# Optimization experiments

Measured on AMD Instinct MI355X. Metric: run time of the kernel, lower is better.

## Reference

```python
import jax, jax.numpy as jnp
import numpy as np

L, B, S, D, H = 4, 4, 2048, 512, 8
DH = D // H
FF = 4 * D
BN_EPS = 1e-3  # keras BatchNormalization default epsilon


def setup_inputs() -> dict:
    key = jax.random.key(0)
    ks = jax.random.split(key, 8)
    g = lambda k, shape: jax.random.normal(k, shape, dtype=jnp.float32) * 0.02
    return {
        "sequence": jax.random.normal(ks[0], (B, S, D), dtype=jnp.float32),
        "wq": g(ks[1], (L, D, D)), "bq": jnp.zeros((L, D), jnp.float32),
        "wk": g(ks[2], (L, D, D)), "bk": jnp.zeros((L, D), jnp.float32),
        "wv": g(ks[3], (L, D, D)), "bv": jnp.zeros((L, D), jnp.float32),
        "wo": g(ks[4], (L, D, D)), "bo": jnp.zeros((L, D), jnp.float32),
        "w1": g(ks[5], (L, D, FF)), "b1": jnp.zeros((L, FF), jnp.float32),
        "w2": g(ks[6], (L, FF, D)), "b2": jnp.zeros((L, D), jnp.float32),
        "g1": jnp.ones((L, D), jnp.float32), "be1": jnp.zeros((L, D), jnp.float32),
        "g2": jnp.ones((L, D), jnp.float32), "be2": jnp.zeros((L, D), jnp.float32),
    }


def reference(sequence, wq, bq, wk, bk, wv, bv, wo, bo, w1, b1, w2, b2, g1, be1, g2, be2):
    # Inference-mode BatchNorm with moving_mean=0, moving_var=1:
    # bn(x) = x / sqrt(1 + eps) * gamma + beta
    bn_inv = 1.0 / jnp.sqrt(jnp.float32(1.0 + BN_EPS))
    scale = 1.0 / jnp.sqrt(jnp.float32(DH))
    x = sequence  # [B, S, D]
    for i in range(L):
        # Batched multi-head self-attention (== the per-position loop concat)
        q = (x @ wq[i] + bq[i]).reshape(B, S, H, DH)
        k = (x @ wk[i] + bk[i]).reshape(B, S, H, DH)
        v = (x @ wv[i] + bv[i]).reshape(B, S, H, DH)
        att = jax.nn.softmax(jnp.einsum('bqhd,bkhd->bhqk', q, k) * scale, axis=-1)
        o = jnp.einsum('bhqk,bkhd->bqhd', att, v).reshape(B, S, D)
        o = o @ wo[i] + bo[i]
        x = (x + o) * bn_inv * g1[i] + be1[i]          # residual + BN
        f = jax.nn.relu(x @ w1[i] + b1[i]) @ w2[i] + b2[i]  # FFN
        x = (x + f) * bn_inv * g2[i] + be2[i]          # residual + BN
    return x
```

## Files before the change

### kernel.cpp

```cpp
#include <hip/hip_runtime.h>
#include <hip/hip_bf16.h>

#define BB   4
#define SS   2048
#define DDIM 512
#define HH   8
#define DHD  64
#define FFD  2048
#define LLN  4
#define NQKV 1536
#define BN_INV 0.9995003747f
#define QSCALE 0.18033688011112042f

typedef __bf16 bf16x8 __attribute__((ext_vector_type(8)));
typedef __bf16 bf16x4 __attribute__((ext_vector_type(4)));
typedef float  f32x4  __attribute__((ext_vector_type(4)));
typedef float  f32x16 __attribute__((ext_vector_type(16)));

__device__ __forceinline__ void gl2lds16(const void* g, void* l) {
  __builtin_amdgcn_global_load_lds((const __attribute__((address_space(1))) void*)g,
                                   (__attribute__((address_space(3))) void*)l, 16, 0, 0);
}

__device__ __forceinline__ unsigned pkbf16(float a, float b) {
  union { __bf16 h[2]; unsigned u; } x;
  x.h[0] = (__bf16)a; x.h[1] = (__bf16)b;
  return x.u;
}

#define SBAR() do { __builtin_amdgcn_s_barrier(); asm volatile("" ::: "memory"); } while (0)

__global__ __launch_bounds__(256) void k_transpose_w(const float* __restrict__ in,
                                                     __bf16* __restrict__ out,
                                                     int R, int C,
                                                     size_t in_zs, size_t out_zs) {
  __shared__ float tile[32][33];
  in += (size_t)blockIdx.z * in_zs;
  out += (size_t)blockIdx.z * out_zs;
  const int c0 = blockIdx.x * 32, r0 = blockIdx.y * 32;
  const int tx = threadIdx.x & 31, ty = threadIdx.x >> 5;
#pragma unroll
  for (int k = 0; k < 4; ++k) {
    int r = ty + k * 8;
    tile[r][tx] = in[(size_t)(r0 + r) * C + (c0 + tx)];
  }
  __syncthreads();
#pragma unroll
  for (int k = 0; k < 4; ++k) {
    int c = ty + k * 8;
    out[(size_t)(c0 + c) * R + (r0 + tx)] = (__bf16)tile[tx][c];
  }
}

__global__ __launch_bounds__(256) void k_bias_fuse(const float* __restrict__ bq,
                                                   const float* __restrict__ bk,
                                                   const float* __restrict__ bv,
                                                   float* __restrict__ out) {
  const int i = blockIdx.x * 256 + threadIdx.x;
  const int l = i / NQKV, j = i - l * NQKV;
  float v = (j < 512) ? bq[l * 512 + j]
          : (j < 1024) ? bk[l * 512 + j - 512]
                       : bv[l * 512 + j - 1024];
  out[i] = v;
}

__global__ __launch_bounds__(256) void k_transpose_v(const __bf16* __restrict__ qkv,
                                                     __bf16* __restrict__ vt) {
  __shared__ __bf16 tile[32][33];
  const int s0 = blockIdx.x * 32;
  const int d0 = blockIdx.y * 32;
  const int bh = blockIdx.z, b = bh >> 3, h = bh & 7;
  const int tx = threadIdx.x & 31, ty = threadIdx.x >> 5;
#pragma unroll
  for (int k = 0; k < 4; ++k) {
    int s = ty + k * 8;
    tile[s][tx] = qkv[(size_t)(b * SS + s0 + s) * NQKV + 2 * DDIM + h * DHD + d0 + tx];
  }
  __syncthreads();
#pragma unroll
  for (int k = 0; k < 4; ++k) {
    int d = ty + k * 8;
    vt[(size_t)(bh * DHD + d0 + d) * SS + (s0 + tx)] = tile[tx][d];
  }
}

__global__ __launch_bounds__(256) void k_cast(const float* __restrict__ in,
                                              float* __restrict__ xf,
                                              __bf16* __restrict__ xb) {
  const int i = (blockIdx.x * 256 + threadIdx.x) * 4;
  const float4 v = *(const float4*)(in + i);
  *(float4*)(xf + i) = v;
  bf16x4 o;
  o[0] = (__bf16)v.x; o[1] = (__bf16)v.y; o[2] = (__bf16)v.z; o[3] = (__bf16)v.w;
  *(bf16x4*)(xb + i) = o;
}

template <int EPI>
__global__ __launch_bounds__(256) void k_gemm_bt(const __bf16* __restrict__ A,
                                                 const __bf16* __restrict__ Bt,
                                                 const float* __restrict__ bias,
                                                 __bf16* __restrict__ Cb,
                                                 int M, int N, int K,
                                                 const float* __restrict__ xres,
                                                 float* __restrict__ xout,
                                                 const float* __restrict__ gvec,
                                                 const float* __restrict__ bvec) {
  __shared__ __align__(16) char As[2][16384];
  __shared__ __align__(16) char Bs[2][16384];
  const int tid = threadIdx.x;
  const int l = tid & 63, w = tid >> 6;
  const int wm = w >> 1, wn = w & 1;
  const int m0 = blockIdx.y * 128, n0 = blockIdx.x * 128;
  const int lr = l & 15, lg = l >> 4;
  f32x4 acc[4][4] = {};
  const int nk = K >> 6;
  const size_t ldab = (size_t)K * 2;

  auto stage = [&](int buf, int kt) {
    const int k0b = kt * 128;
#pragma unroll
    for (int i = 0; i < 4; ++i) {
      const int chunk = i * 256 + tid;
      const int row = chunk >> 3;
      const int scb = ((chunk & 7) * 16) ^ ((row & 7) << 4);
      gl2lds16((const char*)A + (size_t)(m0 + row) * ldab + k0b + scb,
               As[buf] + (i * 256 + w * 64) * 16);
      gl2lds16((const char*)Bt + (size_t)(n0 + row) * ldab + k0b + scb,
               Bs[buf] + (i * 256 + w * 64) * 16);
    }
  };

  stage(0, 0);
  __syncthreads();
  int cur = 0;
  for (int kt = 0; kt < nk; ++kt) {
    if (kt + 1 < nk) stage(cur ^ 1, kt + 1);
#pragma unroll
    for (int kk = 0; kk < 2; ++kk) {
      bf16x8 a[4], b[4];
#pragma unroll
      for (int m = 0; m < 4; ++m) {
        const int row = wm * 64 + m * 16 + lr;
        const int cb = kk * 64 + lg * 16;
        a[m] = *(const bf16x8*)(As[cur] + row * 128 + (cb ^ ((row & 7) << 4)));
      }
#pragma unroll
      for (int n = 0; n < 4; ++n) {
        const int row = wn * 64 + n * 16 + lr;
        const int cb = kk * 64 + lg * 16;
        b[n] = *(const bf16x8*)(Bs[cur] + row * 128 + (cb ^ ((row & 7) << 4)));
      }
#pragma unroll
      for (int m = 0; m < 4; ++m)
#pragma unroll
        for (int n = 0; n < 4; ++n)
          acc[m][n] = __builtin_amdgcn_mfma_f32_16x16x32_bf16(a[m], b[n], acc[m][n], 0, 0, 0);
    }
    asm volatile("s_waitcnt vmcnt(0)" ::: "memory");
    __syncthreads();
    cur ^= 1;
  }
#pragma unroll
  for (int m = 0; m < 4; ++m) {
    const int gm = m0 + wm * 64 + m * 16 + lg * 4;
#pragma unroll
    for (int n = 0; n < 4; ++n) {
      const int gn = n0 + wn * 64 + n * 16 + lr;
      const float bv_ = bias[gn];
#pragma unroll
      for (int j = 0; j < 4; ++j) {
        const size_t idx = (size_t)(gm + j) * N + gn;
        float v = acc[m][n][j] + bv_;
        if constexpr (EPI == 1) {
          Cb[idx] = (__bf16)fmaxf(v, 0.0f);
        } else if constexpr (EPI == 2) {
          float t = (xres[idx] + v) * BN_INV * gvec[gn] + bvec[gn];
          xout[idx] = t;
          Cb[idx] = (__bf16)t;
        } else {
          if (gn < DDIM) v *= QSCALE;
          Cb[idx] = (__bf16)v;
        }
      }
    }
  }
}

template <int EPI>
__global__ __launch_bounds__(512, 1) void k_gemm256(const __bf16* __restrict__ A,
                                                    const __bf16* __restrict__ Bt,
                                                    const float* __restrict__ bias,
                                                    __bf16* __restrict__ Cb,
                                                    int M, int N, int K) {
  __shared__ __align__(16) char As[2][32768];
  __shared__ __align__(16) char Bs[2][32768];
  const int tid = threadIdx.x;
  const int l = tid & 63, w = tid >> 6;
  const int wm = w >> 2, wn = w & 3;
  const int m0 = blockIdx.y * 256, n0 = blockIdx.x * 256;
  const int lr = l & 15, lg = l >> 4;
  f32x4 acc[8][4] = {};
  const int nk = K >> 6;
  const size_t ldab = (size_t)K * 2;

  auto stA = [&](int buf, int kt, int h) {
    const int k0b = kt * 128;
#pragma unroll
    for (int i = 0; i < 2; ++i) {
      const int chunk = h * 1024 + i * 512 + tid;
      const int row = chunk >> 3;
      const int scb = ((chunk & 7) * 16) ^ ((row & 7) << 4);
      gl2lds16((const char*)A + (size_t)(m0 + row) * ldab + k0b + scb,
               As[buf] + (h * 1024 + i * 512 + w * 64) * 16);
    }
  };
  auto stB = [&](int buf, int kt, int h) {
    const int k0b = kt * 128;
#pragma unroll
    for (int i = 0; i < 2; ++i) {
      const int chunk = h * 1024 + i * 512 + tid;
      const int row = chunk >> 3;
      const int scb = ((chunk & 7) * 16) ^ ((row & 7) << 4);
      gl2lds16((const char*)Bt + (size_t)(n0 + row) * ldab + k0b + scb,
               Bs[buf] + (h * 1024 + i * 512 + w * 64) * 16);
    }
  };

  stA(0, 0, 0); stA(0, 0, 1); stB(0, 0, 0); stB(0, 0, 1);
  asm volatile("s_waitcnt vmcnt(0)" ::: "memory");
  SBAR();

  int cur = 0;
  for (int kt = 0; kt < nk; ++kt) {
    const char* Ac = As[cur];
    const char* Bc = Bs[cur];
    const int oth = cur ^ 1;
    const bool pf = (kt + 1 < nk);
    bf16x8 af[4][2], bfr[4][2];
#pragma unroll
    for (int mi = 0; mi < 4; ++mi) {
      const int row = wm * 128 + mi * 16 + lr;
      const int swz = (row & 7) << 4;
#pragma unroll
      for (int kk = 0; kk < 2; ++kk)
        af[mi][kk] = *(const bf16x8*)(Ac + row * 128 + ((kk * 64 + lg * 16) ^ swz));
    }
#pragma unroll
    for (int ni = 0; ni < 2; ++ni) {
      const int row = wn * 64 + ni * 16 + lr;
      const int swz = (row & 7) << 4;
#pragma unroll
      for (int kk = 0; kk < 2; ++kk)
        bfr[ni][kk] = *(const bf16x8*)(Bc + row * 128 + ((kk * 64 + lg * 16) ^ swz));
    }
    if (pf) { stA(oth, kt + 1, 0); stA(oth, kt + 1, 1); }
    SBAR();
    __builtin_amdgcn_s_setprio(1);
#pragma unroll
    for (int mi = 0; mi < 4; ++mi)
#pragma unroll
      for (int ni = 0; ni < 2; ++ni)
#pragma unroll
        for (int kk = 0; kk < 2; ++kk)
          acc[mi][ni] = __builtin_amdgcn_mfma_f32_16x16x32_bf16(af[mi][kk], bfr[ni][kk], acc[mi][ni], 0, 0, 0);
    __builtin_amdgcn_s_setprio(0);
    SBAR();
#pragma unroll
    for (int ni = 2; ni < 4; ++ni) {
      const int row = wn * 64 + ni * 16 + lr;
      const int swz = (row & 7) << 4;
#pragma unroll
      for (int kk = 0; kk < 2; ++kk)
        bfr[ni][kk] = *(const bf16x8*)(Bc + row * 128 + ((kk * 64 + lg * 16) ^ swz));
    }
    if (pf) { stB(oth, kt + 1, 0); stB(oth, kt + 1, 1); }
    SBAR();
    __builtin_amdgcn_s_setprio(1);
#pragma unroll
    for (int mi = 0; mi < 4; ++mi)
#pragma unroll
      for (int ni = 2; ni < 4; ++ni)
#pragma unroll
        for (int kk = 0; kk < 2; ++kk)
          acc[mi][ni] = __builtin_amdgcn_mfma_f32_16x16x32_bf16(af[mi][kk], bfr[ni][kk], acc[mi][ni], 0, 0, 0);
    __builtin_amdgcn_s_setprio(0);
    SBAR();
#pragma unroll
    for (int mi = 0; mi < 4; ++mi) {
      const int row = wm * 128 + (mi + 4) * 16 + lr;
      const int swz = (row & 7) << 4;
#pragma unroll
      for (int kk = 0; kk < 2; ++kk)
        af[mi][kk] = *(const bf16x8*)(Ac + row * 128 + ((kk * 64 + lg * 16) ^ swz));
    }
    SBAR();
    __builtin_amdgcn_s_setprio(1);
#pragma unroll
    for (int mi = 0; mi < 4; ++mi)
#pragma unroll
      for (int ni = 0; ni < 2; ++ni)
#pragma unroll
        for (int kk = 0; kk < 2; ++kk)
          acc[mi + 4][ni] = __builtin_amdgcn_mfma_f32_16x16x32_bf16(af[mi][kk], bfr[ni][kk], acc[mi + 4][ni], 0, 0, 0);
    __builtin_amdgcn_s_setprio(0);
    SBAR();
    __builtin_amdgcn_s_setprio(1);
#pragma unroll
    for (int mi = 0; mi < 4; ++mi)
#pragma unroll
      for (int ni = 2; ni < 4; ++ni)
#pragma unroll
        for (int kk = 0; kk < 2; ++kk)
          acc[mi + 4][ni] = __builtin_amdgcn_mfma_f32_16x16x32_bf16(af[mi][kk], bfr[ni][kk], acc[mi + 4][ni], 0, 0, 0);
    __builtin_amdgcn_s_setprio(0);
    asm volatile("s_waitcnt vmcnt(0)" ::: "memory");
    SBAR();
    cur ^= 1;
  }
#pragma unroll
  for (int mi = 0; mi < 8; ++mi) {
    const int gm = m0 + wm * 128 + mi * 16 + lg * 4;
#pragma unroll
    for (int ni = 0; ni < 4; ++ni) {
      const int gn = n0 + wn * 64 + ni * 16 + lr;
      const float bv_ = bias[gn];
#pragma unroll
      for (int j = 0; j < 4; ++j) {
        const size_t idx = (size_t)(gm + j) * N + gn;
        float v = acc[mi][ni][j] + bv_;
        if constexpr (EPI == 1) {
          Cb[idx] = (__bf16)fmaxf(v, 0.0f);
        } else {
          if (gn < DDIM) v *= QSCALE;
          Cb[idx] = (__bf16)v;
        }
      }
    }
  }
}

__global__ __launch_bounds__(256, 2) void k_attn(const __bf16* __restrict__ QKV,
                                                 const __bf16* __restrict__ Vt,
                                                 __bf16* __restrict__ O) {
  __shared__ char smem[65536];
  const int tid = threadIdx.x, l = tid & 63, w = tid >> 6;
  const int lq = l & 31, hi = l >> 5;
  const int f = blockIdx.y * 16 + blockIdx.x;
  const int L = (f & 7) * 64 + (f >> 3);
  const int qt = L & 15, bh = L >> 4;
  const int b = bh >> 3, h = bh & 7;
  const int myq = qt * 128 + w * 32 + lq;
  bf16x8 qf[4];
  {
    const __bf16* qp = QKV + (size_t)(b * SS + myq) * NQKV + h * DHD + hi * 8;
#pragma unroll
    for (int kc = 0; kc < 4; ++kc)
      qf[kc] = *(const bf16x8*)(qp + kc * 16);
  }
  f32x16 oaccT[2] = {};
  float rsum = 0.f;

  auto stage = [&](int buf, int t) {
    const int kv0 = t * 128;
    char* Kd = smem + buf * 16384;
    char* Vd = smem + 32768 + buf * 16384;
#pragma unroll
    for (int i = 0; i < 4; ++i) {
      const int chunk = i * 256 + tid;
      const int row = chunk >> 3;
      const int rs = row ^ ((((row >> 2) + 1) & 2) * 6);
      const int scb = ((chunk & 7) * 16) ^ ((row & 7) << 4);
      gl2lds16((const char*)QKV + ((size_t)(b * SS + kv0 + rs) * NQKV + DDIM + h * DHD) * 2 + scb,
               Kd + (i * 256 + w * 64) * 16);
    }
#pragma unroll
    for (int i = 0; i < 4; ++i) {
      const int chunk = i * 256 + tid;
      const int row = chunk >> 4;
      const int scb = ((chunk & 15) * 16) ^ ((row & 15) << 4);
      gl2lds16((const char*)Vt + ((size_t)(bh * DHD + row) * SS + kv0) * 2 + scb,
               Vd + (i * 256 + w * 64) * 16);
    }
  };

  stage(0, 0);
  __syncthreads();
  int cur = 0;
  for (int t = 0; t < SS / 128; ++t) {
    if (t < SS / 128 - 1) stage(cur ^ 1, t + 1);
    const char* Ks = smem + cur * 16384;
    const char* Vs = smem + 32768 + cur * 16384;
#pragma unroll
    for (int kt2 = 0; kt2 < 4; ++kt2) {
      const int krow = kt2 * 32 + lq;
      const int kswz = (krow & 7) << 4;
      f32x16 st = {};
      __builtin_amdgcn_s_setprio(1);
#pragma unroll
      for (int kc = 0; kc < 4; ++kc) {
        bf16x8 kf = *(const bf16x8*)(Ks + krow * 128 + ((kc * 32 + hi * 16) ^ kswz));
        st = __builtin_amdgcn_mfma_f32_32x32x16_bf16(kf, qf[kc], st, 0, 0, 0);
      }
      __builtin_amdgcn_s_setprio(0);
      unsigned pk8[8];
#pragma unroll
      for (int i = 0; i < 8; ++i) {
        const float e0 = __builtin_amdgcn_exp2f(st[2 * i]);
        const float e1 = __builtin_amdgcn_exp2f(st[2 * i + 1]);
        rsum += e0 + e1;
        pk8[i] = pkbf16(e0, e1);
      }
      union { unsigned u[4]; bf16x8 v; } pf0, pf1;
#pragma unroll
      for (int i = 0; i < 4; ++i) { pf0.u[i] = pk8[i]; pf1.u[i] = pk8[4 + i]; }
      __builtin_amdgcn_s_setprio(1);
#pragma unroll
      for (int dt = 0; dt < 2; ++dt) {
        const int vrow = dt * 32 + lq;
        const int vswz = (vrow & 15) << 4;
        bf16x8 vf0 = *(const bf16x8*)(Vs + vrow * 256 + ((kt2 * 64 + hi * 16) ^ vswz));
        bf16x8 vf1 = *(const bf16x8*)(Vs + vrow * 256 + ((kt2 * 64 + 32 + hi * 16) ^ vswz));
        oaccT[dt] = __builtin_amdgcn_mfma_f32_32x32x16_bf16(vf0, pf0.v, oaccT[dt], 0, 0, 0);
        oaccT[dt] = __builtin_amdgcn_mfma_f32_32x32x16_bf16(vf1, pf1.v, oaccT[dt], 0, 0, 0);
      }
      __builtin_amdgcn_s_setprio(0);
    }
    asm volatile("s_waitcnt vmcnt(0)" ::: "memory");
    __syncthreads();
    cur ^= 1;
  }
  rsum += __shfl_xor(rsum, 32);
  const float inv = 1.0f / rsum;
  __bf16* op = O + (size_t)(b * SS + myq) * DDIM + h * DHD;
#pragma unroll
  for (int dt = 0; dt < 2; ++dt)
#pragma unroll
    for (int g = 0; g < 4; ++g) {
      const int d0 = dt * 32 + g * 8 + hi * 4;
      unsigned u0 = pkbf16(oaccT[dt][4 * g + 0] * inv, oaccT[dt][4 * g + 1] * inv);
      unsigned u1 = pkbf16(oaccT[dt][4 * g + 2] * inv, oaccT[dt][4 * g + 3] * inv);
      uint2 uu; uu.x = u0; uu.y = u1;
      *(uint2*)(op + d0) = uu;
    }
}

static constexpr size_t SZ_WQKVT = (size_t)LLN * NQKV * DDIM * 2;
static constexpr size_t SZ_WOT   = (size_t)LLN * DDIM * DDIM * 2;
static constexpr size_t SZ_WT_DF = (size_t)LLN * DDIM * FFD * 2;
static constexpr size_t SZ_BQKV  = (size_t)LLN * NQKV * 4;
static constexpr size_t SZ_X     = (size_t)BB * SS * DDIM * 4;
static constexpr size_t SZ_ABF   = (size_t)BB * SS * DDIM * 2;
static constexpr size_t SZ_QKV   = (size_t)BB * SS * NQKV * 2;
static constexpr size_t OFF_WQKVT = 0;
static constexpr size_t OFF_WOT  = OFF_WQKVT + SZ_WQKVT;
static constexpr size_t OFF_W1T  = OFF_WOT + SZ_WOT;
static constexpr size_t OFF_W2T  = OFF_W1T + SZ_WT_DF;
static constexpr size_t OFF_BQKV = OFF_W2T + SZ_WT_DF;
static constexpr size_t OFF_X    = OFF_BQKV + SZ_BQKV;
static constexpr size_t OFF_XB   = OFF_X + SZ_X;
static constexpr size_t OFF_QKV  = OFF_XB + SZ_ABF;
static constexpr size_t OFF_VT   = OFF_QKV + SZ_QKV;
static constexpr size_t OFF_OB   = OFF_VT + SZ_ABF;
static constexpr size_t OFF_H1   = OFF_QKV;

extern "C" void kernel_launch(void* const* d_in, const int* in_sizes, int n_in,
                              void* d_out, int out_size, void* d_ws, size_t ws_size,
                              hipStream_t stream) {
  const float* seq = (const float*)d_in[0];
  const float* wq = (const float*)d_in[1];  const float* bq = (const float*)d_in[2];
  const float* wk = (const float*)d_in[3];  const float* bk = (const float*)d_in[4];
  const float* wv = (const float*)d_in[5];  const float* bv = (const float*)d_in[6];
  const float* wo = (const float*)d_in[7];  const float* bo = (const float*)d_in[8];
  const float* w1 = (const float*)d_in[9];  const float* b1 = (const float*)d_in[10];
  const float* w2 = (const float*)d_in[11]; const float* b2 = (const float*)d_in[12];
  const float* g1 = (const float*)d_in[13]; const float* be1 = (const float*)d_in[14];
  const float* g2 = (const float*)d_in[15]; const float* be2 = (const float*)d_in[16];

  char* ws = (char*)d_ws;
  __bf16* wqkvt = (__bf16*)(ws + OFF_WQKVT);
  __bf16* wot = (__bf16*)(ws + OFF_WOT);
  __bf16* w1t = (__bf16*)(ws + OFF_W1T);
  __bf16* w2t = (__bf16*)(ws + OFF_W2T);
  float*  bqkv = (float*)(ws + OFF_BQKV);
  float*  xf  = (float*)(ws + OFF_X);
  __bf16* xb  = (__bf16*)(ws + OFF_XB);
  __bf16* qkvb = (__bf16*)(ws + OFF_QKV);
  __bf16* vtb = (__bf16*)(ws + OFF_VT);
  __bf16* ob  = (__bf16*)(ws + OFF_OB);
  __bf16* h1  = (__bf16*)(ws + OFF_H1);

  const size_t zDD = (size_t)DDIM * DDIM;
  const size_t zQKV = (size_t)NQKV * DDIM;
  const size_t zDF = (size_t)DDIM * FFD;
  k_transpose_w<<<dim3(16, 16, LLN), 256, 0, stream>>>(wq, wqkvt, DDIM, DDIM, zDD, zQKV);
  k_transpose_w<<<dim3(16, 16, LLN), 256, 0, stream>>>(wk, wqkvt + (size_t)DDIM * DDIM, DDIM, DDIM, zDD, zQKV);
  k_transpose_w<<<dim3(16, 16, LLN), 256, 0, stream>>>(wv, wqkvt + (size_t)2 * DDIM * DDIM, DDIM, DDIM, zDD, zQKV);
  k_transpose_w<<<dim3(16, 16, LLN), 256, 0, stream>>>(wo, wot, DDIM, DDIM, zDD, zDD);
  k_transpose_w<<<dim3(64, 16, LLN), 256, 0, stream>>>(w1, w1t, DDIM, FFD, zDF, zDF);
  k_transpose_w<<<dim3(16, 64, LLN), 256, 0, stream>>>(w2, w2t, FFD, DDIM, zDF, zDF);
  k_bias_fuse<<<LLN * NQKV / 256, 256, 0, stream>>>(bq, bk, bv, bqkv);
  k_cast<<<4096, 256, 0, stream>>>(seq, xf, xb);

  const int M = BB * SS;
  for (int i = 0; i < LLN; ++i) {
    k_gemm256<3><<<dim3(NQKV / 256, M / 256), 512, 0, stream>>>(
        xb, wqkvt + (size_t)i * NQKV * DDIM, bqkv + i * NQKV, qkvb, M, NQKV, DDIM);
    k_transpose_v<<<dim3(SS / 32, DHD / 32, BB * HH), 256, 0, stream>>>(qkvb, vtb);
    k_attn<<<dim3(SS / 128, BB * HH), 256, 0, stream>>>(qkvb, vtb, ob);
    k_gemm_bt<2><<<dim3(DDIM / 128, M / 128), 256, 0, stream>>>(
        ob, wot + (size_t)i * DDIM * DDIM, bo + i * DDIM, xb, M, DDIM, DDIM,
        xf, xf, g1 + i * DDIM, be1 + i * DDIM);
    k_gemm256<1><<<dim3(FFD / 256, M / 256), 512, 0, stream>>>(
        xb, w1t + (size_t)i * DDIM * FFD, b1 + i * FFD, h1, M, FFD, DDIM);
    k_gemm_bt<2><<<dim3(DDIM / 128, M / 128), 256, 0, stream>>>(
        h1, w2t + (size_t)i * DDIM * FFD, b2 + i * DDIM, xb, M, DDIM, FFD,
        xf, (i == LLN - 1) ? (float*)d_out : xf, g2 + i * DDIM, be2 + i * DDIM);
  }
  (void)in_sizes; (void)n_in; (void)out_size; (void)ws_size;
}
```

Baseline: 641.4 us.

## Process two query sub-tiles per wave in attention to reuse K/V fragments

```diff
diff --git a/kernel.cpp b/kernel.cpp
--- a/kernel.cpp
+++ b/kernel.cpp
@@ -339,9 +339,9 @@
   }
 }
 
-__global__ __launch_bounds__(256, 2) void k_attn(const __bf16* __restrict__ QKV,
-                                                 const __bf16* __restrict__ Vt,
-                                                 __bf16* __restrict__ O) {
+__global__ __launch_bounds__(128) void k_attn(const __bf16* __restrict__ QKV,
+                                              const __bf16* __restrict__ Vt,
+                                              __bf16* __restrict__ O) {
   __shared__ char smem[65536];
   const int tid = threadIdx.x, l = tid & 63, w = tid >> 6;
   const int lq = l & 31, hi = l >> 5;
@@ -349,37 +349,38 @@
   const int L = (f & 7) * 64 + (f >> 3);
   const int qt = L & 15, bh = L >> 4;
   const int b = bh >> 3, h = bh & 7;
-  const int myq = qt * 128 + w * 32 + lq;
-  bf16x8 qf[4];
-  {
-    const __bf16* qp = QKV + (size_t)(b * SS + myq) * NQKV + h * DHD + hi * 8;
+  const int q0 = qt * 128 + w * 64;
+  bf16x8 qf[2][4];
+#pragma unroll
+  for (int qh = 0; qh < 2; ++qh) {
+    const __bf16* qp = QKV + (size_t)(b * SS + q0 + qh * 32 + lq) * NQKV + h * DHD + hi * 8;
 #pragma unroll
     for (int kc = 0; kc < 4; ++kc)
-      qf[kc] = *(const bf16x8*)(qp + kc * 16);
-  }
-  f32x16 oaccT[2] = {};
-  float rsum = 0.f;
+      qf[qh][kc] = *(const bf16x8*)(qp + kc * 16);
+  }
+  f32x16 oaccT[2][2] = {};
+  float rsum[2] = {0.f, 0.f};
 
   auto stage = [&](int buf, int t) {
     const int kv0 = t * 128;
     char* Kd = smem + buf * 16384;
     char* Vd = smem + 32768 + buf * 16384;
 #pragma unroll
-    for (int i = 0; i < 4; ++i) {
-      const int chunk = i * 256 + tid;
+    for (int i = 0; i < 8; ++i) {
+      const int chunk = i * 128 + tid;
       const int row = chunk >> 3;
       const int rs = row ^ ((((row >> 2) + 1) & 2) * 6);
       const int scb = ((chunk & 7) * 16) ^ ((row & 7) << 4);
       gl2lds16((const char*)QKV + ((size_t)(b * SS + kv0 + rs) * NQKV + DDIM + h * DHD) * 2 + scb,
-               Kd + (i * 256 + w * 64) * 16);
-    }
-#pragma unroll
-    for (int i = 0; i < 4; ++i) {
-      const int chunk = i * 256 + tid;
+               Kd + (i * 128 + w * 64) * 16);
+    }
+#pragma unroll
+    for (int i = 0; i < 8; ++i) {
+      const int chunk = i * 128 + tid;
       const int row = chunk >> 4;
       const int scb = ((chunk & 15) * 16) ^ ((row & 15) << 4);
       gl2lds16((const char*)Vt + ((size_t)(bh * DHD + row) * SS + kv0) * 2 + scb,
-               Vd + (i * 256 + w * 64) * 16);
+               Vd + (i * 128 + w * 64) * 16);
     }
   };
 
@@ -394,25 +395,29 @@
     for (int kt2 = 0; kt2 < 4; ++kt2) {
       const int krow = kt2 * 32 + lq;
       const int kswz = (krow & 7) << 4;
-      f32x16 st = {};
+      f32x16 st0 = {}, st1 = {};
       __builtin_amdgcn_s_setprio(1);
 #pragma unroll
       for (int kc = 0; kc < 4; ++kc) {
         bf16x8 kf = *(const bf16x8*)(Ks + krow * 128 + ((kc * 32 + hi * 16) ^ kswz));
-        st = __builtin_amdgcn_mfma_f32_32x32x16_bf16(kf, qf[kc], st, 0, 0, 0);
+        st0 = __builtin_amdgcn_mfma_f32_32x32x16_bf16(kf, qf[0][kc], st0, 0, 0, 0);
+        st1 = __builtin_amdgcn_mfma_f32_32x32x16_bf16(kf, qf[1][kc], st1, 0, 0, 0);
       }
       __builtin_amdgcn_s_setprio(0);
-      unsigned pk8[8];
+      union { unsigned u[4]; bf16x8 v; } pf0[2], pf1[2];
 #pragma unroll
       for (int i = 0; i < 8; ++i) {
-        const float e0 = __builtin_amdgcn_exp2f(st[2 * i]);
-        const float e1 = __builtin_amdgcn_exp2f(st[2 * i + 1]);
-        rsum += e0 + e1;
-        pk8[i] = pkbf16(e0, e1);
-      }
-      union { unsigned u[4]; bf16x8 v; } pf0, pf1;
-#pragma unroll
-      for (int i = 0; i < 4; ++i) { pf0.u[i] = pk8[i]; pf1.u[i] = pk8[4 + i]; }
+        const float a0 = __builtin_amdgcn_exp2f(st0[2 * i]);
+        const float a1 = __builtin_amdgcn_exp2f(st0[2 * i + 1]);
+        rsum[0] += a0 + a1;
+        const unsigned ua = pkbf16(a0, a1);
+        if (i < 4) pf0[0].u[i] = ua; else pf1[0].u[i - 4] = ua;
+        const float c0 = __builtin_amdgcn_exp2f(st1[2 * i]);
+        const float c1 = __builtin_amdgcn_exp2f(st1[2 * i + 1]);
+        rsum[1] += c0 + c1;
+        const unsigned uc = pkbf16(c0, c1);
+        if (i < 4) pf0[1].u[i] = uc; else pf1[1].u[i - 4] = uc;
+      }
       __builtin_amdgcn_s_setprio(1);
 #pragma unroll
       for (int dt = 0; dt < 2; ++dt) {
@@ -420,8 +425,11 @@
         const int vswz = (vrow & 15) << 4;
         bf16x8 vf0 = *(const bf16x8*)(Vs + vrow * 256 + ((kt2 * 64 + hi * 16) ^ vswz));
         bf16x8 vf1 = *(const bf16x8*)(Vs + vrow * 256 + ((kt2 * 64 + 32 + hi * 16) ^ vswz));
-        oaccT[dt] = __builtin_amdgcn_mfma_f32_32x32x16_bf16(vf0, pf0.v, oaccT[dt], 0, 0, 0);
-        oaccT[dt] = __builtin_amdgcn_mfma_f32_32x32x16_bf16(vf1, pf1.v, oaccT[dt], 0, 0, 0);
+#pragma unroll
+        for (int qh = 0; qh < 2; ++qh) {
+          oaccT[dt][qh] = __builtin_amdgcn_mfma_f32_32x32x16_bf16(vf0, pf0[qh].v, oaccT[dt][qh], 0, 0, 0);
+          oaccT[dt][qh] = __builtin_amdgcn_mfma_f32_32x32x16_bf16(vf1, pf1[qh].v, oaccT[dt][qh], 0, 0, 0);
+        }
       }
       __builtin_amdgcn_s_setprio(0);
     }
@@ -429,19 +437,23 @@
     __syncthreads();
     cur ^= 1;
   }
-  rsum += __shfl_xor(rsum, 32);
-  const float inv = 1.0f / rsum;
-  __bf16* op = O + (size_t)(b * SS + myq) * DDIM + h * DHD;
-#pragma unroll
-  for (int dt = 0; dt < 2; ++dt)
-#pragma unroll
-    for (int g = 0; g < 4; ++g) {
-      const int d0 = dt * 32 + g * 8 + hi * 4;
-      unsigned u0 = pkbf16(oaccT[dt][4 * g + 0] * inv, oaccT[dt][4 * g + 1] * inv);
-      unsigned u1 = pkbf16(oaccT[dt][4 * g + 2] * inv, oaccT[dt][4 * g + 3] * inv);
-      uint2 uu; uu.x = u0; uu.y = u1;
-      *(uint2*)(op + d0) = uu;
-    }
+#pragma unroll
+  for (int qh = 0; qh < 2; ++qh) {
+    float v = rsum[qh];
+    v += __shfl_xor(v, 32);
+    const float inv = 1.0f / v;
+    __bf16* op = O + (size_t)(b * SS + q0 + qh * 32 + lq) * DDIM + h * DHD;
+#pragma unroll
+    for (int dt = 0; dt < 2; ++dt)
+#pragma unroll
+      for (int g = 0; g < 4; ++g) {
+        const int d0 = dt * 32 + g * 8 + hi * 4;
+        unsigned u0 = pkbf16(oaccT[dt][qh][4 * g + 0] * inv, oaccT[dt][qh][4 * g + 1] * inv);
+        unsigned u1 = pkbf16(oaccT[dt][qh][4 * g + 2] * inv, oaccT[dt][qh][4 * g + 3] * inv);
+        uint2 uu; uu.x = u0; uu.y = u1;
+        *(uint2*)(op + d0) = uu;
+      }
+  }
 }
 
 static constexpr size_t SZ_WQKVT = (size_t)LLN * NQKV * DDIM * 2;
@@ -506,7 +518,7 @@
     k_gemm256<3><<<dim3(NQKV / 256, M / 256), 512, 0, stream>>>(
         xb, wqkvt + (size_t)i * NQKV * DDIM, bqkv + i * NQKV, qkvb, M, NQKV, DDIM);
     k_transpose_v<<<dim3(SS / 32, DHD / 32, BB * HH), 256, 0, stream>>>(qkvb, vtb);
-    k_attn<<<dim3(SS / 128, BB * HH), 256, 0, stream>>>(qkvb, vtb, ob);
+    k_attn<<<dim3(SS / 128, BB * HH), 128, 0, stream>>>(qkvb, vtb, ob);
     k_gemm_bt<2><<<dim3(DDIM / 128, M / 128), 256, 0, stream>>>(
         ob, wot + (size_t)i * DDIM * DDIM, bo + i * DDIM, xb, M, DDIM, DDIM,
         xf, xf, g1 + i * DDIM, be1 + i * DDIM);
```

After: 684.2 us. 6.7% more time.

## Single-buffer K tile in attention to fit three blocks per CU

Applied to the files above, without the earlier changes.

```diff
diff --git a/kernel.cpp b/kernel.cpp
--- a/kernel.cpp
+++ b/kernel.cpp
@@ -339,10 +339,10 @@
   }
 }
 
-__global__ __launch_bounds__(256, 2) void k_attn(const __bf16* __restrict__ QKV,
+__global__ __launch_bounds__(256, 3) void k_attn(const __bf16* __restrict__ QKV,
                                                  const __bf16* __restrict__ Vt,
                                                  __bf16* __restrict__ O) {
-  __shared__ char smem[65536];
+  __shared__ char smem[49152];
   const int tid = threadIdx.x, l = tid & 63, w = tid >> 6;
   const int lq = l & 31, hi = l >> 5;
   const int f = blockIdx.y * 16 + blockIdx.x;
@@ -360,10 +360,8 @@
   f32x16 oaccT[2] = {};
   float rsum = 0.f;
 
-  auto stage = [&](int buf, int t) {
+  auto stageK = [&](int t) {
     const int kv0 = t * 128;
-    char* Kd = smem + buf * 16384;
-    char* Vd = smem + 32768 + buf * 16384;
 #pragma unroll
     for (int i = 0; i < 4; ++i) {
       const int chunk = i * 256 + tid;
@@ -371,8 +369,12 @@
       const int rs = row ^ ((((row >> 2) + 1) & 2) * 6);
       const int scb = ((chunk & 7) * 16) ^ ((row & 7) << 4);
       gl2lds16((const char*)QKV + ((size_t)(b * SS + kv0 + rs) * NQKV + DDIM + h * DHD) * 2 + scb,
-               Kd + (i * 256 + w * 64) * 16);
-    }
+               smem + (i * 256 + w * 64) * 16);
+    }
+  };
+  auto stageV = [&](int buf, int t) {
+    const int kv0 = t * 128;
+    char* Vd = smem + 16384 + buf * 16384;
 #pragma unroll
     for (int i = 0; i < 4; ++i) {
       const int chunk = i * 256 + tid;
@@ -383,36 +385,41 @@
     }
   };
 
-  stage(0, 0);
-  __syncthreads();
-  int cur = 0;
+  stageK(0); stageV(0, 0);
+  asm volatile("s_waitcnt vmcnt(0)" ::: "memory");
+  SBAR();
+  int vcur = 0;
   for (int t = 0; t < SS / 128; ++t) {
-    if (t < SS / 128 - 1) stage(cur ^ 1, t + 1);
-    const char* Ks = smem + cur * 16384;
-    const char* Vs = smem + 32768 + cur * 16384;
+    const char* Vs = smem + 16384 + vcur * 16384;
+    f32x16 st[4];
+    __builtin_amdgcn_s_setprio(1);
 #pragma unroll
     for (int kt2 = 0; kt2 < 4; ++kt2) {
       const int krow = kt2 * 32 + lq;
       const int kswz = (krow & 7) << 4;
-      f32x16 st = {};
-      __builtin_amdgcn_s_setprio(1);
+      f32x16 z = {};
 #pragma unroll
       for (int kc = 0; kc < 4; ++kc) {
-        bf16x8 kf = *(const bf16x8*)(Ks + krow * 128 + ((kc * 32 + hi * 16) ^ kswz));
-        st = __builtin_amdgcn_mfma_f32_32x32x16_bf16(kf, qf[kc], st, 0, 0, 0);
-      }
-      __builtin_amdgcn_s_setprio(0);
-      unsigned pk8[8];
+        bf16x8 kf = *(const bf16x8*)(smem + krow * 128 + ((kc * 32 + hi * 16) ^ kswz));
+        z = __builtin_amdgcn_mfma_f32_32x32x16_bf16(kf, qf[kc], z, 0, 0, 0);
+      }
+      st[kt2] = z;
+    }
+    __builtin_amdgcn_s_setprio(0);
+    asm volatile("s_waitcnt vmcnt(0)" ::: "memory");
+    SBAR();
+    if (t + 1 < SS / 128) { stageK(t + 1); stageV(vcur ^ 1, t + 1); }
+#pragma unroll
+    for (int kt2 = 0; kt2 < 4; ++kt2) {
+      union { unsigned u[4]; bf16x8 v; } pf0, pf1;
 #pragma unroll
       for (int i = 0; i < 8; ++i) {
-        const float e0 = __builtin_amdgcn_exp2f(st[2 * i]);
-        const float e1 = __builtin_amdgcn_exp2f(st[2 * i + 1]);
+        const float e0 = __builtin_amdgcn_exp2f(st[kt2][2 * i]);
+        const float e1 = __builtin_amdgcn_exp2f(st[kt2][2 * i + 1]);
         rsum += e0 + e1;
-        pk8[i] = pkbf16(e0, e1);
-      }
-      union { unsigned u[4]; bf16x8 v; } pf0, pf1;
-#pragma unroll
-      for (int i = 0; i < 4; ++i) { pf0.u[i] = pk8[i]; pf1.u[i] = pk8[4 + i]; }
+        const unsigned u = pkbf16(e0, e1);
+        if (i < 4) pf0.u[i] = u; else pf1.u[i - 4] = u;
+      }
       __builtin_amdgcn_s_setprio(1);
 #pragma unroll
       for (int dt = 0; dt < 2; ++dt) {
@@ -425,9 +432,11 @@
       }
       __builtin_amdgcn_s_setprio(0);
     }
-    asm volatile("s_waitcnt vmcnt(0)" ::: "memory");
-    __syncthreads();
-    cur ^= 1;
+    if (t + 1 < SS / 128) {
+      asm volatile("s_waitcnt vmcnt(4)" ::: "memory");
+    }
+    SBAR();
+    vcur ^= 1;
   }
   rsum += __shfl_xor(rsum, 32);
   const float inv = 1.0f / rsum;
```

New measurement: 651.3 us. About the same (+1.5%).

## Fuse V transpose into QKV GEMM epilogue and keep residual stream in bf16

Applied to the files above, without the earlier changes.

```diff
diff --git a/kernel.cpp b/kernel.cpp
--- a/kernel.cpp
+++ b/kernel.cpp
@@ -64,32 +64,10 @@
   out[i] = v;
 }
 
-__global__ __launch_bounds__(256) void k_transpose_v(const __bf16* __restrict__ qkv,
-                                                     __bf16* __restrict__ vt) {
-  __shared__ __bf16 tile[32][33];
-  const int s0 = blockIdx.x * 32;
-  const int d0 = blockIdx.y * 32;
-  const int bh = blockIdx.z, b = bh >> 3, h = bh & 7;
-  const int tx = threadIdx.x & 31, ty = threadIdx.x >> 5;
-#pragma unroll
-  for (int k = 0; k < 4; ++k) {
-    int s = ty + k * 8;
-    tile[s][tx] = qkv[(size_t)(b * SS + s0 + s) * NQKV + 2 * DDIM + h * DHD + d0 + tx];
-  }
-  __syncthreads();
-#pragma unroll
-  for (int k = 0; k < 4; ++k) {
-    int d = ty + k * 8;
-    vt[(size_t)(bh * DHD + d0 + d) * SS + (s0 + tx)] = tile[tx][d];
-  }
-}
-
 __global__ __launch_bounds__(256) void k_cast(const float* __restrict__ in,
-                                              float* __restrict__ xf,
                                               __bf16* __restrict__ xb) {
   const int i = (blockIdx.x * 256 + threadIdx.x) * 4;
   const float4 v = *(const float4*)(in + i);
-  *(float4*)(xf + i) = v;
   bf16x4 o;
   o[0] = (__bf16)v.x; o[1] = (__bf16)v.y; o[2] = (__bf16)v.z; o[3] = (__bf16)v.w;
   *(bf16x4*)(xb + i) = o;
@@ -99,9 +77,9 @@
 __global__ __launch_bounds__(256) void k_gemm_bt(const __bf16* __restrict__ A,
                                                  const __bf16* __restrict__ Bt,
                                                  const float* __restrict__ bias,
-                                                 __bf16* __restrict__ Cb,
+                                                 __bf16* Cb,
                                                  int M, int N, int K,
-                                                 const float* __restrict__ xres,
+                                                 const __bf16* xres,
                                                  float* __restrict__ xout,
                                                  const float* __restrict__ gvec,
                                                  const float* __restrict__ bvec) {
@@ -173,13 +151,10 @@
         float v = acc[m][n][j] + bv_;
         if constexpr (EPI == 1) {
           Cb[idx] = (__bf16)fmaxf(v, 0.0f);
-        } else if constexpr (EPI == 2) {
-          float t = (xres[idx] + v) * BN_INV * gvec[gn] + bvec[gn];
-          xout[idx] = t;
+        } else {
+          float t = ((float)xres[idx] + v) * BN_INV * gvec[gn] + bvec[gn];
+          if (xout) xout[idx] = t;
           Cb[idx] = (__bf16)t;
-        } else {
-          if (gn < DDIM) v *= QSCALE;
-          Cb[idx] = (__bf16)v;
         }
       }
     }
@@ -191,7 +166,8 @@
                                                     const __bf16* __restrict__ Bt,
                                                     const float* __restrict__ bias,
                                                     __bf16* __restrict__ Cb,
-                                                    int M, int N, int K) {
+                                                    int M, int N, int K,
+                                                    __bf16* __restrict__ vt) {
   __shared__ __align__(16) char As[2][32768];
   __shared__ __align__(16) char Bs[2][32768];
   const int tid = threadIdx.x;
@@ -317,23 +293,39 @@
     SBAR();
     cur ^= 1;
   }
+  const int bidx = m0 >> 11;
 #pragma unroll
   for (int mi = 0; mi < 8; ++mi) {
     const int gm = m0 + wm * 128 + mi * 16 + lg * 4;
 #pragma unroll
     for (int ni = 0; ni < 4; ++ni) {
-      const int gn = n0 + wn * 64 + ni * 16 + lr;
+      const int gnb = n0 + wn * 64 + ni * 16;
+      const int gn = gnb + lr;
       const float bv_ = bias[gn];
-#pragma unroll
-      for (int j = 0; j < 4; ++j) {
-        const size_t idx = (size_t)(gm + j) * N + gn;
-        float v = acc[mi][ni][j] + bv_;
-        if constexpr (EPI == 1) {
-          Cb[idx] = (__bf16)fmaxf(v, 0.0f);
-        } else {
-          if (gn < DDIM) v *= QSCALE;
-          Cb[idx] = (__bf16)v;
+      if (EPI == 1 || gnb < 2 * DDIM) {
+#pragma unroll
+        for (int j = 0; j < 4; ++j) {
+          const size_t idx = (size_t)(gm + j) * N + gn;
+          float v = acc[mi][ni][j] + bv_;
+          if constexpr (EPI == 1) {
+            Cb[idx] = (__bf16)fmaxf(v, 0.0f);
+          } else {
+            if (gn < DDIM) v *= QSCALE;
+            Cb[idx] = (__bf16)v;
+          }
         }
+      } else {
+        const int d = gn - 2 * DDIM;
+        const int h = d >> 6, dh = d & 63;
+        const int sbase = gm & 2047;
+        const float v0 = acc[mi][ni][0] + bv_;
+        const float v1 = acc[mi][ni][1] + bv_;
+        const float v2 = acc[mi][ni][2] + bv_;
+        const float v3 = acc[mi][ni][3] + bv_;
+        uint2 uu;
+        uu.x = pkbf16(v0, v1);
+        uu.y = pkbf16(v2, v3);
+        *(uint2*)(vt + ((size_t)((bidx * 8 + h) * 64 + dh)) * SS + sbase) = uu;
       }
     }
   }
@@ -448,7 +440,6 @@
 static constexpr size_t SZ_WOT   = (size_t)LLN * DDIM * DDIM * 2;
 static constexpr size_t SZ_WT_DF = (size_t)LLN * DDIM * FFD * 2;
 static constexpr size_t SZ_BQKV  = (size_t)LLN * NQKV * 4;
-static constexpr size_t SZ_X     = (size_t)BB * SS * DDIM * 4;
 static constexpr size_t SZ_ABF   = (size_t)BB * SS * DDIM * 2;
 static constexpr size_t SZ_QKV   = (size_t)BB * SS * NQKV * 2;
 static constexpr size_t OFF_WQKVT = 0;
@@ -456,8 +447,7 @@
 static constexpr size_t OFF_W1T  = OFF_WOT + SZ_WOT;
 static constexpr size_t OFF_W2T  = OFF_W1T + SZ_WT_DF;
 static constexpr size_t OFF_BQKV = OFF_W2T + SZ_WT_DF;
-static constexpr size_t OFF_X    = OFF_BQKV + SZ_BQKV;
-static constexpr size_t OFF_XB   = OFF_X + SZ_X;
+static constexpr size_t OFF_XB   = OFF_BQKV + SZ_BQKV;
 static constexpr size_t OFF_QKV  = OFF_XB + SZ_ABF;
 static constexpr size_t OFF_VT   = OFF_QKV + SZ_QKV;
 static constexpr size_t OFF_OB   = OFF_VT + SZ_ABF;
@@ -482,7 +472,6 @@
   __bf16* w1t = (__bf16*)(ws + OFF_W1T);
   __bf16* w2t = (__bf16*)(ws + OFF_W2T);
   float*  bqkv = (float*)(ws + OFF_BQKV);
-  float*  xf  = (float*)(ws + OFF_X);
   __bf16* xb  = (__bf16*)(ws + OFF_XB);
   __bf16* qkvb = (__bf16*)(ws + OFF_QKV);
   __bf16* vtb = (__bf16*)(ws + OFF_VT);
@@ -499,22 +488,21 @@
   k_transpose_w<<<dim3(64, 16, LLN), 256, 0, stream>>>(w1, w1t, DDIM, FFD, zDF, zDF);
   k_transpose_w<<<dim3(16, 64, LLN), 256, 0, stream>>>(w2, w2t, FFD, DDIM, zDF, zDF);
   k_bias_fuse<<<LLN * NQKV / 256, 256, 0, stream>>>(bq, bk, bv, bqkv);
-  k_cast<<<4096, 256, 0, stream>>>(seq, xf, xb);
+  k_cast<<<4096, 256, 0, stream>>>(seq, xb);
 
   const int M = BB * SS;
   for (int i = 0; i < LLN; ++i) {
     k_gemm256<3><<<dim3(NQKV / 256, M / 256), 512, 0, stream>>>(
-        xb, wqkvt + (size_t)i * NQKV * DDIM, bqkv + i * NQKV, qkvb, M, NQKV, DDIM);
-    k_transpose_v<<<dim3(SS / 32, DHD / 32, BB * HH), 256, 0, stream>>>(qkvb, vtb);
+        xb, wqkvt + (size_t)i * NQKV * DDIM, bqkv + i * NQKV, qkvb, M, NQKV, DDIM, vtb);
     k_attn<<<dim3(SS / 128, BB * HH), 256, 0, stream>>>(qkvb, vtb, ob);
     k_gemm_bt<2><<<dim3(DDIM / 128, M / 128), 256, 0, stream>>>(
         ob, wot + (size_t)i * DDIM * DDIM, bo + i * DDIM, xb, M, DDIM, DDIM,
-        xf, xf, g1 + i * DDIM, be1 + i * DDIM);
+        xb, nullptr, g1 + i * DDIM, be1 + i * DDIM);
     k_gemm256<1><<<dim3(FFD / 256, M / 256), 512, 0, stream>>>(
-        xb, w1t + (size_t)i * DDIM * FFD, b1 + i * FFD, h1, M, FFD, DDIM);
+        xb, w1t + (size_t)i * DDIM * FFD, b1 + i * FFD, h1, M, FFD, DDIM, nullptr);
     k_gemm_bt<2><<<dim3(DDIM / 128, M / 128), 256, 0, stream>>>(
         h1, w2t + (size_t)i * DDIM * FFD, b2 + i * DDIM, xb, M, DDIM, FFD,
-        xf, (i == LLN - 1) ? (float*)d_out : xf, g2 + i * DDIM, be2 + i * DDIM);
+        xb, (i == LLN - 1) ? (float*)d_out : nullptr, g2 + i * DDIM, be2 + i * DDIM);
   }
   (void)in_sizes; (void)n_in; (void)out_size; (void)ws_size;
 }
```

Result: slower. 690.2 us (+7.6%).
